# Kernel tuning notes

Measured on AMD Instinct MI355X. Metric: run time of the kernel, lower is better.

Reference implementation:

```python
import jax, jax.numpy as jnp
import numpy as np

N_NODES = 10000
N_EDGES = 320000
NUM_NEIGHBORS = 32.0
INV_SQRT3 = 1.0 / np.sqrt(3.0)  # component-normalized CG for 1o x 1o -> 0e


def setup_inputs() -> dict:
    key = jax.random.key(0)
    ks = jax.random.split(key, 16)
    f32 = jnp.float32
    return {
        "node_input": jax.random.normal(ks[0], (N_NODES, 160), f32),   # 64x0e | 32x1o
        "node_attr": jnp.ones((N_NODES, 1), f32),                       # 1x0e
        "edge_attr": jax.random.normal(ks[1], (N_EDGES, 4), f32),       # 1x0e | 1x1o (sph harm)
        "edge_scalar_attr": jax.random.normal(ks[2], (N_EDGES, 8), f32),# radial basis
        "Wsc0": jax.random.normal(ks[3], (64, 64), f32),
        "Wsc1": jax.random.normal(ks[4], (32, 32), f32),
        "Wl1_0": jax.random.normal(ks[5], (64, 64), f32),
        "Wl1_1": jax.random.normal(ks[6], (32, 32), f32),
        "Wfc1": jax.random.normal(ks[7], (8, 64), f32),
        "Wfc2": jax.random.normal(ks[8], (64, 64), f32),
        "Wfc3": jax.random.normal(ks[9], (64, 192), f32),  # -> tp.weight_numel
        "Wl2_s": jax.random.normal(ks[10], (96, 64), f32),
        "Wl2_v": jax.random.normal(ks[11], (96, 32), f32),
        "Wa": jax.random.normal(ks[12], (96, 1), f32),
        "edge_src": jax.random.randint(ks[13], (N_EDGES,), 0, N_NODES),
        "edge_dst": jax.random.randint(ks[14], (N_EDGES,), 0, N_NODES),
    }


def _fctp_scalar_attr(xs, xv, Ws, Wv, a):
    """FullyConnectedTensorProduct(irreps, '0e', irreps) with scalar node attr a.
    xs: [N, mul_s] scalars, xv: [N, mul_v, 3] vectors. Path-normalized by 1/sqrt(fan_in)."""
    out_s = (xs @ Ws) * (a / np.sqrt(xs.shape[1]))[:, None]
    out_v = jnp.einsum('nuc,uw->nwc', xv, Wv) * (a / np.sqrt(xv.shape[1]))[:, None, None]
    return out_s, out_v


def reference(node_input, node_attr, edge_attr, edge_scalar_attr,
              Wsc0, Wsc1, Wl1_0, Wl1_1, Wfc1, Wfc2, Wfc3, Wl2_s, Wl2_v, Wa,
              edge_src, edge_dst):
    N = node_input.shape[0]
    a = node_attr[:, 0]                              # [N] scalar attr
    xs = node_input[:, :64]                          # [N,64]  64x0e
    xv = node_input[:, 64:].reshape(N, 32, 3)        # [N,32,3] 32x1o

    # self connection: FCTp(input, attr, output)
    sc_s, sc_v = _fctp_scalar_attr(xs, xv, Wsc0, Wsc1, a)
    # lin1: FCTp(input, attr, input)
    f_s, f_v = _fctp_scalar_attr(xs, xv, Wl1_0, Wl1_1, a)

    # radial MLP -> tensor-product weights [E, 192]
    h = jax.nn.gelu(edge_scalar_attr @ Wfc1 / np.sqrt(8.0))
    h = jax.nn.gelu(h @ Wfc2 / np.sqrt(64.0))
    w = h @ Wfc3 / np.sqrt(64.0)
    w0, w1, w2, w3 = w[:, :64], w[:, 64:128], w[:, 128:160], w[:, 160:192]

    # gather source node features per edge
    gs = f_s[edge_src]                               # [E,64]
    gv = f_v[edge_src]                               # [E,32,3]
    y0 = edge_attr[:, 0]                             # [E]   0e
    y1 = edge_attr[:, 1:4]                           # [E,3] 1o

    # 'uvu' tensor product, irreps_mid (sorted) = 64x0e + 32x0e + 64x1o + 32x1o
    mid0 = w0 * gs * y0[:, None]                                        # 0e x 0e -> 0e
    mid1 = w3 * jnp.einsum('euc,ec->eu', gv, y1) * INV_SQRT3            # 1o x 1o -> 0e
    mid2 = (w1 * gs)[:, :, None] * y1[:, None, :]                       # 0e x 1o -> 1o
    mid3 = w2[:, :, None] * gv * y0[:, None, None]                      # 1o x 0e -> 1o

    # scatter-add to destination nodes, normalized by sqrt(num_neighbors)
    inv = 1.0 / np.sqrt(NUM_NEIGHBORS)
    seg = lambda x: jax.ops.segment_sum(x, edge_dst, num_segments=N) * inv
    ns0, ns1, nv2, nv3 = seg(mid0), seg(mid1), seg(mid2), seg(mid3)

    mid_s = jnp.concatenate([ns0, ns1], axis=1)      # [N,96] scalars of irreps_mid
    mid_v = jnp.concatenate([nv2, nv3], axis=1)      # [N,96,3] vectors of irreps_mid

    # lin2: FCTp(mid, attr, output), fan_in = 96 for both scalar and vector outputs
    out_s = (mid_s @ Wl2_s) * (a / np.sqrt(96.0))[:, None]
    out_v = jnp.einsum('nuc,uw->nwc', mid_v, Wl2_v) * (a / np.sqrt(96.0))[:, None, None]

    # alpha: FCTp(mid, attr, '0e'); self_con output_mask is all ones here
    alpha = (mid_s @ Wa) * (a / np.sqrt(96.0))[:, None]  # [N,1]

    res_s = sc_s + alpha * out_s
    res_v = sc_v + alpha[:, :, None] * out_v
    return jnp.concatenate([res_s, res_v.reshape(N, 96)], axis=1)  # [N,160]
```

## Files before the change

### kernel.cpp

```cpp
#include <hip/hip_runtime.h>

#define N_NODES 10000
#define N_EDGES 320000
#define INV3 0.5773502691896258f

typedef short short8 __attribute__((ext_vector_type(8)));
typedef float f32x4 __attribute__((ext_vector_type(4)));

__device__ __forceinline__ float gelu_f(float x) {
    float x3 = x * x * x;
    float e = __expf(-1.5957691216057308f * (x + 0.044715f * x3));
    return x * __builtin_amdgcn_rcpf(1.0f + e);
}

__device__ __forceinline__ unsigned short f2bf(float f) {
    unsigned u = __float_as_uint(f);
    unsigned r = (u + 0x7FFFu + ((u >> 16) & 1u)) >> 16;
    return (unsigned short)r;
}
__device__ __forceinline__ float bf2f(unsigned short u) {
    return __uint_as_float(((unsigned)u) << 16);
}
__device__ __forceinline__ unsigned pk2(unsigned short lo, unsigned short hi) {
    return (unsigned)lo | ((unsigned)hi << 16);
}

__device__ __forceinline__ float rowsum16(float v) {
    v += __int_as_float(__builtin_amdgcn_update_dpp(0, __float_as_int(v), 0x118, 0xf, 0xf, true));
    v += __int_as_float(__builtin_amdgcn_update_dpp(0, __float_as_int(v), 0x114, 0xf, 0xf, true));
    v += __int_as_float(__builtin_amdgcn_update_dpp(0, __float_as_int(v), 0x112, 0xf, 0xf, true));
    v += __int_as_float(__builtin_amdgcn_update_dpp(0, __float_as_int(v), 0x111, 0xf, 0xf, true));
    return v;
}

__global__ __launch_bounds__(256) void pre_kernel(
    const int* __restrict__ edge_dst, int* __restrict__ deg,
    const float* __restrict__ Wfc1, const float* __restrict__ Wfc2,
    const float* __restrict__ Wfc3, uint4* __restrict__ fragbuf,
    const float* __restrict__ node_input, const float* __restrict__ node_attr,
    const float* __restrict__ Wl1_0, const float* __restrict__ Wl1_1,
    unsigned short* __restrict__ f_sb, unsigned short* __restrict__ f_vb)
{
    const int b = blockIdx.x;
    if (b < 1250) {
        int e = b * 256 + threadIdx.x;
        if (e < N_EDGES) atomicAdd(&deg[edge_dst[e]], 1);
        return;
    }
    if (b < 1259) {
        const int tile = (b - 1250) * 4 + (threadIdx.x >> 6);
        if (tile >= 36) return;
        const int l = threadIdx.x & 63;
        const int e = l & 15, g = l >> 4;
        unsigned p[4] = {0u, 0u, 0u, 0u};
        if (tile < 4) {
            if (g == 0) {
                #pragma unroll
                for (int j = 0; j < 8; ++j) {
                    unsigned short bb = f2bf(Wfc1[j * 64 + tile * 16 + e]);
                    p[j >> 1] |= (unsigned)bb << (16 * (j & 1));
                }
            }
        } else if (tile < 12) {
            int t2 = tile - 4; int mt = t2 >> 1, kt = t2 & 1;
            #pragma unroll
            for (int j = 0; j < 8; ++j) {
                unsigned short bb = f2bf(Wfc2[(kt * 32 + g * 8 + j) * 64 + mt * 16 + e]);
                p[j >> 1] |= (unsigned)bb << (16 * (j & 1));
            }
        } else {
            int t3 = tile - 12; int mt3 = t3 >> 1, kt = t3 & 1;
            #pragma unroll
            for (int j = 0; j < 8; ++j) {
                unsigned short bb = f2bf(Wfc3[(kt * 32 + g * 8 + j) * 192 + mt3 * 16 + e]);
                p[j >> 1] |= (unsigned)bb << (16 * (j & 1));
            }
        }
        uint4 v; v.x = p[0]; v.y = p[1]; v.z = p[2]; v.w = p[3];
        fragbuf[tile * 64 + l] = v;
        return;
    }
    const int wid = threadIdx.x >> 6;
    const int t = threadIdx.x & 63;
    const int n = (b - 1259) * 4 + wid;
    __shared__ float x[4][160];
    const float* row = node_input + (size_t)n * 160;
    for (int i = t; i < 160; i += 64) x[wid][i] = row[i];
    const float a = node_attr[n];

    float acc = 0.f;
    for (int k = 0; k < 64; ++k) acc += x[wid][k] * Wl1_0[k * 64 + t];
    f_sb[(size_t)n * 64 + t] = f2bf(acc * (a * 0.125f));

    const float sv = a * 0.17677669529663687f;
    for (int o = t; o < 96; o += 64) {
        int w = o / 3, c = o - w * 3;
        float av = 0.f;
        for (int u = 0; u < 32; ++u) av += x[wid][64 + u * 3 + c] * Wl1_1[u * 32 + w];
        f_vb[(size_t)n * 96 + o] = f2bf(av * sv);
    }
}

__global__ __launch_bounds__(256) void alloc_kernel(const int* __restrict__ deg,
                                                    int* __restrict__ gctr,
                                                    int* __restrict__ rowptr,
                                                    int* __restrict__ cursor) {
    int n = blockIdx.x * 256 + threadIdx.x;
    if (n < N_NODES) {
        int d = deg[n];
        int base = atomicAdd(gctr, d);
        rowptr[n] = base;
        cursor[n] = base;
    }
}

__global__ __launch_bounds__(256) void scatter_kernel(const int* __restrict__ dst,
                                                      int* __restrict__ cursor,
                                                      int* __restrict__ elist) {
    int e = blockIdx.x * 256 + threadIdx.x;
    if (e < N_EDGES) {
        int p = atomicAdd(&cursor[dst[e]], 1);
        elist[p] = e;
    }
}

#define L3CHUNK(mt3_, d_) { \
    short8 a0_ = ((short8*)wfrag)[(12 + (mt3_) * 2 + 0) * 64 + l]; \
    short8 a1_ = ((short8*)wfrag)[(12 + (mt3_) * 2 + 1) * 64 + l]; \
    d_[0] = 0.f; d_[1] = 0.f; d_[2] = 0.f; d_[3] = 0.f; \
    d_ = __builtin_amdgcn_mfma_f32_16x16x32_bf16(a0_, bh0, d_, 0, 0, 0); \
    d_ = __builtin_amdgcn_mfma_f32_16x16x32_bf16(a1_, bh1, d_, 0, 0, 0); }

__global__ __launch_bounds__(256) __attribute__((amdgpu_waves_per_eu(2, 4)))
void fused_kernel(
    const float* __restrict__ edge_attr,
    const float* __restrict__ esa,
    const unsigned short* __restrict__ f_sb,
    const unsigned short* __restrict__ f_vb,
    const int* __restrict__ edge_src,
    const int* __restrict__ elist,
    const int* __restrict__ rowptr,
    const int* __restrict__ deg,
    const float4* __restrict__ fragbuf,
    const float* __restrict__ node_input,
    const float* __restrict__ node_attr,
    const float* __restrict__ Wsc0,
    const float* __restrict__ Wsc1,
    const float* __restrict__ Wl2_s,
    const float* __restrict__ Wl2_v,
    const float* __restrict__ Wa,
    float* __restrict__ out)
{
    __shared__ __align__(16) char wfrag[36864];
    __shared__ __align__(16) char albuf[4 * 2048];
    __shared__ __align__(16) float xld[2][160];

    const int tid = threadIdx.x;
    const int l = tid & 63;
    const int wid = tid >> 6;
    const int q = wid & 1;
    const int ns = wid >> 1;

    {
        float4* w = (float4*)wfrag;
        #pragma unroll
        for (int i = 0; i < 9; ++i) w[tid + 256 * i] = fragbuf[tid + 256 * i];
    }

    const int n = blockIdx.x * 2 + ns;
    const int p0 = rowptr[n], p1 = p0 + deg[n];

    if (q == 0)
        for (int i = l; i < 160; i += 64) xld[ns][i] = node_input[(size_t)n * 160 + i];

    __syncthreads();

    const int er = l & 15, gr = l >> 4;
    const int swz = (er & 7) << 4;
    char* al = albuf + wid * 2048;

    float acc0[2][4];
    float acc1[4];
    float acc2[2][4][3];
    float acc3[4][3];
    #pragma unroll
    for (int jj = 0; jj < 2; ++jj)
        #pragma unroll
        for (int r = 0; r < 4; ++r) {
            acc0[jj][r] = 0.f;
            acc2[jj][r][0] = 0.f; acc2[jj][r][1] = 0.f; acc2[jj][r][2] = 0.f;
        }
    #pragma unroll
    for (int r = 0; r < 4; ++r) {
        acc1[r] = 0.f;
        acc3[r][0] = 0.f; acc3[r][1] = 0.f; acc3[r][2] = 0.f;
    }

    float4 ea = {0.f, 0.f, 0.f, 0.f};
    int src = 0;
    uint4 bxu = {0u, 0u, 0u, 0u};
    if (p0 < p1) {
        const int ci = p0 + er;
        const bool cv = ci < p1;
        const int ec = elist[cv ? ci : p0];
        ea = ((const float4*)edge_attr)[ec];
        src = edge_src[ec];
        if (l < 16 && cv) {
            float4 xa = ((const float4*)esa)[(size_t)ec * 2 + 0];
            float4 xb = ((const float4*)esa)[(size_t)ec * 2 + 1];
            bxu.x = pk2(f2bf(xa.x), f2bf(xa.y));
            bxu.y = pk2(f2bf(xa.z), f2bf(xa.w));
            bxu.z = pk2(f2bf(xb.x), f2bf(xb.y));
            bxu.w = pk2(f2bf(xb.z), f2bf(xb.w));
        }
    }

    #pragma unroll 1
    for (int p = p0; p < p1; p += 16) {
        const float y0 = ea.x, y1a = ea.y, y1b = ea.z, y1c = ea.w;
        union { uint4 u; short8 s; } bxc; bxc.u = bxu;
        const short8 bx = bxc.s;
        const int csrc = src;

        ushort4 gsu0 = *(const ushort4*)(f_sb + (size_t)csrc * 64 + (q * 2 + 0) * 16 + gr * 4);
        ushort4 gsu1 = *(const ushort4*)(f_sb + (size_t)csrc * 64 + (q * 2 + 1) * 16 + gr * 4);
        const unsigned short* gvp = f_vb + (size_t)csrc * 96 + (size_t)(q * 16 + gr * 4) * 3;
        ushort4 ga = *(const ushort4*)(gvp + 0);
        ushort4 gb = *(const ushort4*)(gvp + 4);
        ushort4 gc = *(const ushort4*)(gvp + 8);

        {
            const int np = p + 16;
            const bool nv = np + er < p1;
            const int nec = elist[nv ? np + er : p0];
            float4 nea = ((const float4*)edge_attr)[nec];
            int nsrc = edge_src[nec];
            uint4 nbxu = {0u, 0u, 0u, 0u};
            if (l < 16 && nv) {
                float4 xa = ((const float4*)esa)[(size_t)nec * 2 + 0];
                float4 xb = ((const float4*)esa)[(size_t)nec * 2 + 1];
                nbxu.x = pk2(f2bf(xa.x), f2bf(xa.y));
                nbxu.y = pk2(f2bf(xa.z), f2bf(xa.w));
                nbxu.z = pk2(f2bf(xb.x), f2bf(xb.y));
                nbxu.w = pk2(f2bf(xb.z), f2bf(xb.w));
            }
            ea = nea; src = nsrc; bxu = nbxu;
        }

        #pragma unroll
        for (int mt = 0; mt < 4; ++mt) {
            short8 aw = ((short8*)wfrag)[mt * 64 + l];
            f32x4 c = {0.f, 0.f, 0.f, 0.f};
            c = __builtin_amdgcn_mfma_f32_16x16x32_bf16(aw, bx, c, 0, 0, 0);
            unsigned pa = pk2(f2bf(gelu_f(c[0] * 0.35355339059327373f)),
                              f2bf(gelu_f(c[1] * 0.35355339059327373f)));
            unsigned pb = pk2(f2bf(gelu_f(c[2] * 0.35355339059327373f)),
                              f2bf(gelu_f(c[3] * 0.35355339059327373f)));
            uint2 pv; pv.x = pa; pv.y = pb;
            *(uint2*)(al + ((er * 128 + mt * 32 + gr * 8) ^ swz)) = pv;
        }
        {
            short8 b0 = *(short8*)(al + ((er * 128 + 0  + gr * 16) ^ swz));
            short8 b1 = *(short8*)(al + ((er * 128 + 64 + gr * 16) ^ swz));
            #pragma unroll
            for (int mt = 0; mt < 4; ++mt) {
                short8 w2a = ((short8*)(wfrag + 4096))[(2 * mt + 0) * 64 + l];
                short8 w2b = ((short8*)(wfrag + 4096))[(2 * mt + 1) * 64 + l];
                f32x4 c = {0.f, 0.f, 0.f, 0.f};
                c = __builtin_amdgcn_mfma_f32_16x16x32_bf16(w2a, b0, c, 0, 0, 0);
                c = __builtin_amdgcn_mfma_f32_16x16x32_bf16(w2b, b1, c, 0, 0, 0);
                unsigned pa = pk2(f2bf(gelu_f(c[0] * 0.125f)), f2bf(gelu_f(c[1] * 0.125f)));
                unsigned pb = pk2(f2bf(gelu_f(c[2] * 0.125f)), f2bf(gelu_f(c[3] * 0.125f)));
                uint2 pv; pv.x = pa; pv.y = pb;
                *(uint2*)(al + ((er * 128 + mt * 32 + gr * 8) ^ swz)) = pv;
            }
        }
        short8 bh0 = *(short8*)(al + ((er * 128 + 0  + gr * 16) ^ swz));
        short8 bh1 = *(short8*)(al + ((er * 128 + 64 + gr * 16) ^ swz));

        #pragma unroll
        for (int jj = 0; jj < 2; ++jj) {
            const int jg = q * 2 + jj;
            ushort4 gsu = jj ? gsu1 : gsu0;
            f32x4 gs4 = {bf2f(gsu.x), bf2f(gsu.y), bf2f(gsu.z), bf2f(gsu.w)};
            f32x4 dA; L3CHUNK(jg, dA);
            f32x4 dB; L3CHUNK(jg + 4, dB);
            #pragma unroll
            for (int r = 0; r < 4; ++r) {
                acc0[jj][r] += 0.125f * dA[r] * gs4[r] * y0;
                float t_ = 0.125f * dB[r] * gs4[r];
                acc2[jj][r][0] += t_ * y1a;
                acc2[jj][r][1] += t_ * y1b;
                acc2[jj][r][2] += t_ * y1c;
            }
        }
        {
            const int jv = q;
            float gv[12] = {bf2f(ga.x), bf2f(ga.y), bf2f(ga.z), bf2f(ga.w),
                            bf2f(gb.x), bf2f(gb.y), bf2f(gb.z), bf2f(gb.w),
                            bf2f(gc.x), bf2f(gc.y), bf2f(gc.z), bf2f(gc.w)};
            f32x4 dC; L3CHUNK(8 + jv, dC);
            f32x4 dD; L3CHUNK(10 + jv, dD);
            #pragma unroll
            for (int r = 0; r < 4; ++r) {
                float w2v = 0.125f * dC[r] * y0;
                acc3[r][0] += w2v * gv[r * 3 + 0];
                acc3[r][1] += w2v * gv[r * 3 + 1];
                acc3[r][2] += w2v * gv[r * 3 + 2];
                float dot = gv[r * 3 + 0] * y1a + gv[r * 3 + 1] * y1b + gv[r * 3 + 2] * y1c;
                acc1[r] += 0.125f * dD[r] * dot * INV3;
            }
        }
    }

    #pragma unroll
    for (int jj = 0; jj < 2; ++jj)
        #pragma unroll
        for (int r = 0; r < 4; ++r) {
            acc0[jj][r] = rowsum16(acc0[jj][r]);
            acc2[jj][r][0] = rowsum16(acc2[jj][r][0]);
            acc2[jj][r][1] = rowsum16(acc2[jj][r][1]);
            acc2[jj][r][2] = rowsum16(acc2[jj][r][2]);
        }
    #pragma unroll
    for (int r = 0; r < 4; ++r) {
        acc1[r] = rowsum16(acc1[r]);
        acc3[r][0] = rowsum16(acc3[r][0]);
        acc3[r][1] = rowsum16(acc3[r][1]);
        acc3[r][2] = rowsum16(acc3[r][2]);
    }

    __syncthreads();

    float* m = (float*)(albuf + ns * 4096);
    const float iN = 0.17677669529663687f;
    if (er == 15) {
        #pragma unroll
        for (int jj = 0; jj < 2; ++jj) {
            const int jg = q * 2 + jj;
            f32x4 v;
            v[0] = acc0[jj][0] * iN; v[1] = acc0[jj][1] * iN;
            v[2] = acc0[jj][2] * iN; v[3] = acc0[jj][3] * iN;
            *(f32x4*)(m + jg * 16 + gr * 4) = v;
        }
        {
            const int jv = q;
            f32x4 v;
            v[0] = acc1[0] * iN; v[1] = acc1[1] * iN;
            v[2] = acc1[2] * iN; v[3] = acc1[3] * iN;
            *(f32x4*)(m + 64 + jv * 16 + gr * 4) = v;
        }
        #pragma unroll
        for (int jj = 0; jj < 2; ++jj) {
            const int jg = q * 2 + jj;
            float t[12];
            #pragma unroll
            for (int r = 0; r < 4; ++r) {
                t[r * 3 + 0] = acc2[jj][r][0] * iN;
                t[r * 3 + 1] = acc2[jj][r][1] * iN;
                t[r * 3 + 2] = acc2[jj][r][2] * iN;
            }
            float* b = m + 96 + (jg * 16 + gr * 4) * 3;
            *(f32x4*)(b + 0) = (f32x4){t[0], t[1], t[2], t[3]};
            *(f32x4*)(b + 4) = (f32x4){t[4], t[5], t[6], t[7]};
            *(f32x4*)(b + 8) = (f32x4){t[8], t[9], t[10], t[11]};
        }
        {
            const int jv = q;
            float t[12];
            #pragma unroll
            for (int r = 0; r < 4; ++r) {
                t[r * 3 + 0] = acc3[r][0] * iN;
                t[r * 3 + 1] = acc3[r][1] * iN;
                t[r * 3 + 2] = acc3[r][2] * iN;
            }
            float* b = m + 288 + (jv * 16 + gr * 4) * 3;
            *(f32x4*)(b + 0) = (f32x4){t[0], t[1], t[2], t[3]};
            *(f32x4*)(b + 4) = (f32x4){t[4], t[5], t[6], t[7]};
            *(f32x4*)(b + 8) = (f32x4){t[8], t[9], t[10], t[11]};
        }
    }

    __syncthreads();

    const float a = node_attr[n];
    const float* x = xld[ns];
    const float s96 = a * 0.10206207261596575f;

    float alpha = 0.f;
    for (int i = 0; i < 96; ++i) alpha += m[i] * Wa[i];
    alpha *= s96;

    if (q == 0) {
        float outs = 0.f;
        for (int i = 0; i < 96; ++i) outs += m[i] * Wl2_s[i * 64 + l];
        outs *= s96;
        float scs = 0.f;
        for (int k = 0; k < 64; ++k) scs += x[k] * Wsc0[k * 64 + l];
        scs *= a * 0.125f;
        out[(size_t)n * 160 + l] = scs + alpha * outs;
    } else {
        const float sv = a * 0.17677669529663687f;
        for (int o = l; o < 96; o += 64) {
            int w = o / 3, c = o - w * 3;
            float ov = 0.f;
            for (int u = 0; u < 64; ++u) ov += m[96 + u * 3 + c] * Wl2_v[u * 32 + w];
            for (int u = 0; u < 32; ++u) ov += m[288 + u * 3 + c] * Wl2_v[(64 + u) * 32 + w];
            ov *= s96;
            float scv = 0.f;
            for (int u = 0; u < 32; ++u) scv += x[64 + u * 3 + c] * Wsc1[u * 32 + w];
            scv *= sv;
            out[(size_t)n * 160 + 64 + o] = scv + alpha * ov;
        }
    }
}

extern "C" void kernel_launch(void* const* d_in, const int* in_sizes, int n_in,
                              void* d_out, int out_size, void* d_ws, size_t ws_size,
                              hipStream_t stream) {
    const float* node_input = (const float*)d_in[0];
    const float* node_attr  = (const float*)d_in[1];
    const float* edge_attr  = (const float*)d_in[2];
    const float* esa        = (const float*)d_in[3];
    const float* Wsc0       = (const float*)d_in[4];
    const float* Wsc1       = (const float*)d_in[5];
    const float* Wl1_0      = (const float*)d_in[6];
    const float* Wl1_1      = (const float*)d_in[7];
    const float* Wfc1       = (const float*)d_in[8];
    const float* Wfc2       = (const float*)d_in[9];
    const float* Wfc3       = (const float*)d_in[10];
    const float* Wl2_s      = (const float*)d_in[11];
    const float* Wl2_v      = (const float*)d_in[12];
    const float* Wa         = (const float*)d_in[13];
    const int* edge_src     = (const int*)d_in[14];
    const int* edge_dst     = (const int*)d_in[15];
    float* out = (float*)d_out;

    float* ws  = (float*)d_ws;
    unsigned short* f_sb = (unsigned short*)ws;
    unsigned short* f_vb = (unsigned short*)(ws + 320000);
    uint4* fragbuf = (uint4*)(ws + 1600000);
    int* ibuf   = (int*)(ws + 1609216);
    int* deg    = ibuf;
    int* gctr   = ibuf + 10000;
    int* rowptr = ibuf + 10016;
    int* cursor = ibuf + 20032;
    int* elist  = ibuf + 30080;

    hipMemsetAsync(deg, 0, (size_t)(N_NODES + 1) * sizeof(int), stream);

    pre_kernel<<<3759, 256, 0, stream>>>(edge_dst, deg, Wfc1, Wfc2, Wfc3, fragbuf,
                                         node_input, node_attr, Wl1_0, Wl1_1, f_sb, f_vb);
    alloc_kernel<<<(N_NODES + 255) / 256, 256, 0, stream>>>(deg, gctr, rowptr, cursor);
    scatter_kernel<<<(N_EDGES + 255) / 256, 256, 0, stream>>>(edge_dst, cursor, elist);

    fused_kernel<<<N_NODES / 2, 256, 0, stream>>>(edge_attr, esa, f_sb, f_vb,
                                                  edge_src, elist, rowptr, deg,
                                                  (const float4*)fragbuf,
                                                  node_input, node_attr,
                                                  Wsc0, Wsc1, Wl2_s, Wl2_v, Wa,
                                                  out);
}
```

Before: 213.9 us.

## Sort nodes by degree bucket and split MLP layers across wave pairs

```diff
diff --git a/kernel.cpp b/kernel.cpp
--- a/kernel.cpp
+++ b/kernel.cpp
@@ -104,20 +104,44 @@
 __global__ __launch_bounds__(256) void alloc_kernel(const int* __restrict__ deg,
                                                     int* __restrict__ gctr,
                                                     int* __restrict__ rowptr,
-                                                    int* __restrict__ cursor) {
+                                                    int* __restrict__ cursor,
+                                                    int* __restrict__ bcnt) {
     int n = blockIdx.x * 256 + threadIdx.x;
     if (n < N_NODES) {
         int d = deg[n];
         int base = atomicAdd(gctr, d);
         rowptr[n] = base;
         cursor[n] = base;
-    }
-}
-
-__global__ __launch_bounds__(256) void scatter_kernel(const int* __restrict__ dst,
-                                                      int* __restrict__ cursor,
-                                                      int* __restrict__ elist) {
-    int e = blockIdx.x * 256 + threadIdx.x;
+        int nt = (d + 15) >> 4; if (nt > 63) nt = 63;
+        atomicAdd(&bcnt[nt], 1);
+    }
+}
+
+__global__ __launch_bounds__(64) void bscan_kernel(const int* __restrict__ bcnt,
+                                                   int* __restrict__ bcur) {
+    if (threadIdx.x == 0) {
+        int run = 0;
+        for (int i = 63; i >= 0; --i) { bcur[i] = run; run += bcnt[i]; }
+    }
+}
+
+__global__ __launch_bounds__(256) void post_kernel(const int* __restrict__ dst,
+                                                   const int* __restrict__ deg,
+                                                   int* __restrict__ cursor,
+                                                   int* __restrict__ elist,
+                                                   int* __restrict__ bcur,
+                                                   int* __restrict__ nodeperm) {
+    const int b = blockIdx.x;
+    if (b < 40) {
+        int n = b * 256 + threadIdx.x;
+        if (n < N_NODES) {
+            int nt = (deg[n] + 15) >> 4; if (nt > 63) nt = 63;
+            int pos = atomicAdd(&bcur[nt], 1);
+            nodeperm[pos] = n;
+        }
+        return;
+    }
+    int e = (b - 40) * 256 + threadIdx.x;
     if (e < N_EDGES) {
         int p = atomicAdd(&cursor[dst[e]], 1);
         elist[p] = e;
@@ -141,6 +165,7 @@
     const int* __restrict__ elist,
     const int* __restrict__ rowptr,
     const int* __restrict__ deg,
+    const int* __restrict__ nodeperm,
     const float4* __restrict__ fragbuf,
     const float* __restrict__ node_input,
     const float* __restrict__ node_attr,
@@ -152,7 +177,7 @@
     float* __restrict__ out)
 {
     __shared__ __align__(16) char wfrag[36864];
-    __shared__ __align__(16) char albuf[4 * 2048];
+    __shared__ __align__(16) char albuf[2 * 4096];
     __shared__ __align__(16) float xld[2][160];
 
     const int tid = threadIdx.x;
@@ -167,8 +192,14 @@
         for (int i = 0; i < 9; ++i) w[tid + 256 * i] = fragbuf[tid + 256 * i];
     }
 
-    const int n = blockIdx.x * 2 + ns;
-    const int p0 = rowptr[n], p1 = p0 + deg[n];
+    const int n0 = nodeperm[blockIdx.x * 2 + 0];
+    const int n1 = nodeperm[blockIdx.x * 2 + 1];
+    const int n = ns ? n1 : n0;
+    const int dn0 = deg[n0], dn1 = deg[n1];
+    const int ntmax = ((dn0 > dn1 ? dn0 : dn1) + 15) >> 4;
+    const int p0 = rowptr[n];
+    const int p1 = p0 + (ns ? dn1 : dn0);
+    const int p0c = p0 < N_EDGES ? p0 : N_EDGES - 1;
 
     if (q == 0)
         for (int i = l; i < 160; i += 64) xld[ns][i] = node_input[(size_t)n * 160 + i];
@@ -177,7 +208,8 @@
 
     const int er = l & 15, gr = l >> 4;
     const int swz = (er & 7) << 4;
-    char* al = albuf + wid * 2048;
+    char* h1b = albuf + ns * 4096;
+    char* h2b = h1b + 2048;
 
     float acc0[2][4];
     float acc1[4];
@@ -199,10 +231,10 @@
     float4 ea = {0.f, 0.f, 0.f, 0.f};
     int src = 0;
     uint4 bxu = {0u, 0u, 0u, 0u};
-    if (p0 < p1) {
+    if (ntmax > 0) {
         const int ci = p0 + er;
         const bool cv = ci < p1;
-        const int ec = elist[cv ? ci : p0];
+        const int ec = elist[cv ? ci : p0c];
         ea = ((const float4*)edge_attr)[ec];
         src = edge_src[ec];
         if (l < 16 && cv) {
@@ -216,7 +248,7 @@
     }
 
     #pragma unroll 1
-    for (int p = p0; p < p1; p += 16) {
+    for (int it = 0; it < ntmax; ++it) {
         const float y0 = ea.x, y1a = ea.y, y1b = ea.z, y1c = ea.w;
         union { uint4 u; short8 s; } bxc; bxc.u = bxu;
         const short8 bx = bxc.s;
@@ -230,9 +262,9 @@
         ushort4 gc = *(const ushort4*)(gvp + 8);
 
         {
-            const int np = p + 16;
-            const bool nv = np + er < p1;
-            const int nec = elist[nv ? np + er : p0];
+            const int np = p0 + (it + 1) * 16;
+            const bool nv = (np + er) < p1;
+            const int nec = elist[nv ? np + er : p0c];
             float4 nea = ((const float4*)edge_attr)[nec];
             int nsrc = edge_src[nec];
             uint4 nbxu = {0u, 0u, 0u, 0u};
@@ -248,7 +280,8 @@
         }
 
         #pragma unroll
-        for (int mt = 0; mt < 4; ++mt) {
+        for (int j = 0; j < 2; ++j) {
+            const int mt = q * 2 + j;
             short8 aw = ((short8*)wfrag)[mt * 64 + l];
             f32x4 c = {0.f, 0.f, 0.f, 0.f};
             c = __builtin_amdgcn_mfma_f32_16x16x32_bf16(aw, bx, c, 0, 0, 0);
@@ -257,13 +290,15 @@
             unsigned pb = pk2(f2bf(gelu_f(c[2] * 0.35355339059327373f)),
                               f2bf(gelu_f(c[3] * 0.35355339059327373f)));
             uint2 pv; pv.x = pa; pv.y = pb;
-            *(uint2*)(al + ((er * 128 + mt * 32 + gr * 8) ^ swz)) = pv;
-        }
+            *(uint2*)(h1b + ((er * 128 + mt * 32 + gr * 8) ^ swz)) = pv;
+        }
+        __syncthreads();
         {
-            short8 b0 = *(short8*)(al + ((er * 128 + 0  + gr * 16) ^ swz));
-            short8 b1 = *(short8*)(al + ((er * 128 + 64 + gr * 16) ^ swz));
-            #pragma unroll
-            for (int mt = 0; mt < 4; ++mt) {
+            short8 b0 = *(short8*)(h1b + ((er * 128 + 0  + gr * 16) ^ swz));
+            short8 b1 = *(short8*)(h1b + ((er * 128 + 64 + gr * 16) ^ swz));
+            #pragma unroll
+            for (int j = 0; j < 2; ++j) {
+                const int mt = q * 2 + j;
                 short8 w2a = ((short8*)(wfrag + 4096))[(2 * mt + 0) * 64 + l];
                 short8 w2b = ((short8*)(wfrag + 4096))[(2 * mt + 1) * 64 + l];
                 f32x4 c = {0.f, 0.f, 0.f, 0.f};
@@ -272,11 +307,12 @@
                 unsigned pa = pk2(f2bf(gelu_f(c[0] * 0.125f)), f2bf(gelu_f(c[1] * 0.125f)));
                 unsigned pb = pk2(f2bf(gelu_f(c[2] * 0.125f)), f2bf(gelu_f(c[3] * 0.125f)));
                 uint2 pv; pv.x = pa; pv.y = pb;
-                *(uint2*)(al + ((er * 128 + mt * 32 + gr * 8) ^ swz)) = pv;
-            }
-        }
-        short8 bh0 = *(short8*)(al + ((er * 128 + 0  + gr * 16) ^ swz));
-        short8 bh1 = *(short8*)(al + ((er * 128 + 64 + gr * 16) ^ swz));
+                *(uint2*)(h2b + ((er * 128 + mt * 32 + gr * 8) ^ swz)) = pv;
+            }
+        }
+        __syncthreads();
+        short8 bh0 = *(short8*)(h2b + ((er * 128 + 0  + gr * 16) ^ swz));
+        short8 bh1 = *(short8*)(h2b + ((er * 128 + 64 + gr * 16) ^ swz));
 
         #pragma unroll
         for (int jj = 0; jj < 2; ++jj) {
@@ -440,22 +476,28 @@
     unsigned short* f_sb = (unsigned short*)ws;
     unsigned short* f_vb = (unsigned short*)(ws + 320000);
     uint4* fragbuf = (uint4*)(ws + 1600000);
-    int* ibuf   = (int*)(ws + 1609216);
-    int* deg    = ibuf;
-    int* gctr   = ibuf + 10000;
-    int* rowptr = ibuf + 10016;
-    int* cursor = ibuf + 20032;
-    int* elist  = ibuf + 30080;
+    int* ibuf     = (int*)(ws + 1609216);
+    int* deg      = ibuf;
+    int* gctr     = ibuf + 10000;
+    int* rowptr   = ibuf + 10016;
+    int* cursor   = ibuf + 20032;
+    int* elist    = ibuf + 30080;
+    int* bcnt     = ibuf + 350080;
+    int* bcur     = ibuf + 350144;
+    int* nodeperm = ibuf + 350208;
 
     hipMemsetAsync(deg, 0, (size_t)(N_NODES + 1) * sizeof(int), stream);
+    hipMemsetAsync(bcnt, 0, 64 * sizeof(int), stream);
 
     pre_kernel<<<3759, 256, 0, stream>>>(edge_dst, deg, Wfc1, Wfc2, Wfc3, fragbuf,
                                          node_input, node_attr, Wl1_0, Wl1_1, f_sb, f_vb);
-    alloc_kernel<<<(N_NODES + 255) / 256, 256, 0, stream>>>(deg, gctr, rowptr, cursor);
-    scatter_kernel<<<(N_EDGES + 255) / 256, 256, 0, stream>>>(edge_dst, cursor, elist);
+    alloc_kernel<<<(N_NODES + 255) / 256, 256, 0, stream>>>(deg, gctr, rowptr, cursor, bcnt);
+    bscan_kernel<<<1, 64, 0, stream>>>(bcnt, bcur);
+    post_kernel<<<40 + (N_EDGES + 255) / 256, 256, 0, stream>>>(edge_dst, deg, cursor,
+                                                                elist, bcur, nodeperm);
 
     fused_kernel<<<N_NODES / 2, 256, 0, stream>>>(edge_attr, esa, f_sb, f_vb,
-                                                  edge_src, elist, rowptr, deg,
+                                                  edge_src, elist, rowptr, deg, nodeperm,
                                                   (const float4*)fragbuf,
                                                   node_input, node_attr,
                                                   Wsc0, Wsc1, Wl2_s, Wl2_v, Wa,
```

Result: slower. 318.9 us (+49.1%).
